# Performance work log

Hardware: AMD Instinct MI355X
Metric: run time of the kernel (lower is better)

## Reference

```python
import jax, jax.numpy as jnp
import numpy as np

R, N, F, H, C = 3, 100000, 256, 128, 2
N0, S1, D1, S2, D2 = 16384, 16384, 4096, 4096, 512


def setup_inputs() -> dict:
    key = jax.random.key(0)
    ks = jax.random.split(key, 13)
    return {
        "features": jax.random.normal(ks[0], (N, F), jnp.float32),
        "src_nodes": jax.random.randint(ks[1], (R, N0), 0, N),
        "dstsrc2src1": jax.random.randint(ks[2], (R, S1), 0, N0),
        "dstsrc2dst1": jax.random.randint(ks[3], (R, D1), 0, N0),
        "dif_mat1": jax.random.uniform(ks[4], (R, D1, S1), jnp.float32) / S1,
        "dstsrc2src2": jax.random.randint(ks[5], (R, S2), 0, D1),
        "dstsrc2dst2": jax.random.randint(ks[6], (R, D2), 0, D1),
        "dif_mat2": jax.random.uniform(ks[7], (R, D2, S2), jnp.float32) / S2,
        "w1": jax.random.normal(ks[8], (2 * F, H), jnp.float32) * 0.05,
        "w2": jax.random.normal(ks[9], (2 * H, H), jnp.float32) * 0.05,
        "relation_vectors": jax.random.uniform(ks[10], (R, H), jnp.float32),
        "attention_vec": jax.random.uniform(ks[11], (2 * H, 1), jnp.float32),
        "classifier_w": jax.random.normal(ks[12], (H, C), jnp.float32) * 0.05,
    }


def _agg(x, d2s, d2d, dif, w, rel_vec, att_vec):
    # x: [n, din]; dif: [d, s]; w: [2*din, H]
    agg = dif @ x[d2s]                                  # mean-diffused neighbor feats [d, din]
    h = jnp.concatenate([agg, x[d2d]], axis=1) @ w      # [d, H]
    rel = jnp.broadcast_to(rel_vec[None, :], (h.shape[0], rel_vec.shape[0]))
    score = (jnp.concatenate([h, rel], axis=1) @ att_vec)[:, 0]  # [d]
    att = jax.nn.softmax(score)                         # softmax over batch nodes
    return h * att[:, None]


def reference(features, src_nodes, dstsrc2src1, dstsrc2dst1, dif_mat1,
              dstsrc2src2, dstsrc2dst2, dif_mat2, w1, w2,
              relation_vectors, attention_vec, classifier_w):
    def per_relation(src, s1, d1, m1, s2, d2, m2, rel_vec):
        x = features[src]                               # gather node feats [N0, F]
        x = _agg(x, s1, d1, m1, w1, rel_vec, attention_vec)   # [D1, H]
        x = _agg(x, s2, d2, m2, w2, rel_vec, attention_vec)   # [D2, H]
        return x

    xs = jax.vmap(per_relation)(src_nodes, dstsrc2src1, dstsrc2dst1, dif_mat1,
                                dstsrc2src2, dstsrc2dst2, dif_mat2, relation_vectors)
    summed = jnp.sum(xs, axis=0)                        # sum over relations [D2, H]
    inv_norm = jax.lax.rsqrt(jnp.maximum(jnp.sum(summed * summed, axis=1, keepdims=True), 1e-12))
    normed = summed * inv_norm                          # tf.nn.l2_normalize(axis=1)
    return jax.nn.softmax(normed @ classifier_w, axis=-1)
```

## Files before the change

### kernel.cpp

```cpp
#include <hip/hip_runtime.h>
#include <hip/hip_bf16.h>
#include <math.h>

constexpr int Rc  = 3;
constexpr int Fc  = 256;
constexpr int Hc  = 128;
constexpr int N0c = 16384;
constexpr int S1c = 16384;
constexpr int D1c = 4096;
constexpr int S2c = 4096;
constexpr int D2c = 512;
constexpr int KH1 = 4;
constexpr int KH2 = 16;

typedef __bf16 bf16x8 __attribute__((ext_vector_type(8)));
typedef __bf16 bf16x4 __attribute__((ext_vector_type(4)));
typedef float  f32x4  __attribute__((ext_vector_type(4)));

__device__ __forceinline__ void glds16(const void* g, void* l) {
  __builtin_amdgcn_global_load_lds(
      (const __attribute__((address_space(1))) void*)g,
      (__attribute__((address_space(3))) void*)l, 16, 0, 0);
}

__device__ __forceinline__ bf16x8 cvt2(const float4 a, const float4 b) {
  bf16x8 c;
  c[0] = (__bf16)a.x; c[1] = (__bf16)a.y; c[2] = (__bf16)a.z; c[3] = (__bf16)a.w;
  c[4] = (__bf16)b.x; c[5] = (__bf16)b.y; c[6] = (__bf16)b.z; c[7] = (__bf16)b.w;
  return c;
}

__device__ __forceinline__ unsigned short bfbits(float v) {
  __bf16 b = (__bf16)v; unsigned short u;
  __builtin_memcpy(&u, &b, 2); return u;
}

__global__ __launch_bounds__(256, 2)
void wpack(const float* __restrict__ w1, const float* __restrict__ w2,
           unsigned char* __restrict__ wp, float* __restrict__ esum) {
  const int tile = blockIdx.x, half = blockIdx.y, t = threadIdx.x;
  if (tile == 0 && half == 0 && t < 8) esum[t] = 0.f;
  const float* src; int row0;
  if (tile < 4)       { src = w1; row0 = tile * 64; }
  else if (tile < 8)  { src = w1; row0 = 256 + (tile - 4) * 64; }
  else if (tile < 10) { src = w2; row0 = (tile - 8) * 64; }
  else                { src = w2; row0 = 128 + (tile - 10) * 64; }
  unsigned char* dst = wp + ((size_t)half * 12 + tile) * 16384;
  __shared__ float sm[64][132];
  {
    const int r = t >> 2, c0 = (t & 3) * 32;
#pragma unroll
    for (int j = 0; j < 8; j++)
      *(float4*)&sm[r][c0 + 4 * j] = *(const float4*)(src + (size_t)(row0 + r) * 128 + c0 + 4 * j);
  }
  __syncthreads();
  if (t < 128) {
    const int n = t;
#pragma unroll
    for (int ch = 0; ch < 8; ch++) {
      bf16x8 o;
#pragma unroll
      for (int e = 0; e < 8; e++) {
        float v = sm[ch * 8 + e][n];
        __bf16 h = (__bf16)v;
        o[e] = half ? (__bf16)(v - (float)h) : h;
      }
      *(bf16x8*)(dst + n * 128 + ((ch ^ (n & 7)) * 16)) = o;
    }
  }
}

__global__ __launch_bounds__(256, 3)
void gg0(const float* __restrict__ feat, const int* __restrict__ srcn,
         const int* __restrict__ d2s1, const unsigned char* __restrict__ wp,
         unsigned char* __restrict__ xgwp) {
  const int rel = blockIdx.y, bx = blockIdx.x, s0 = bx * 64;
  const unsigned char* Bh = wp;
  const unsigned char* Bl = wp + (size_t)12 * 16384;

  const int t = threadIdx.x, lane = t & 63, w = t >> 6;
  const int mh = w >> 1, nh = w & 1;

  __shared__ __bf16 Asm[64 * 64];
  __shared__ __bf16 Bhs[128 * 64];
  __shared__ __bf16 Bls[128 * 64];

  const int arow = t >> 2, ak0 = (t & 3) * 16;
  const int row = s0 + arow;
  const size_t arowg = (size_t)srcn[rel * N0c + d2s1[(size_t)rel * S1c + row]];
  const float* aptr = feat + arowg * Fc + ak0;
  const int ac0 = ak0 >> 3;
  __bf16* asw0 = &Asm[arow * 64 + ((ac0    ) ^ (arow & 7)) * 8];
  __bf16* asw1 = &Asm[arow * 64 + ((ac0 + 1) ^ (arow & 7)) * 8];

  float4 a[16];
#pragma unroll
  for (int tl = 0; tl < 4; tl++)
#pragma unroll
    for (int j = 0; j < 4; j++) a[tl * 4 + j] = *(const float4*)(aptr + tl * 64 + 4 * j);

  f32x4 acc[2][4] = {};

  for (int tl = 0; tl < 4; ++tl) {
    asm volatile("s_waitcnt lgkmcnt(0)" ::: "memory");
    __builtin_amdgcn_s_barrier();
    __builtin_amdgcn_sched_barrier(0);
    {
      const unsigned char* bh = Bh + (size_t)tl * 16384 + w * 4096 + lane * 16;
      const unsigned char* bl = Bl + (size_t)tl * 16384 + w * 4096 + lane * 16;
      char* dh = (char*)Bhs + w * 4096;
      char* dl = (char*)Bls + w * 4096;
#pragma unroll
      for (int i = 0; i < 4; i++) glds16(bh + i * 1024, dh + i * 1024);
#pragma unroll
      for (int i = 0; i < 4; i++) glds16(bl + i * 1024, dl + i * 1024);
    }
    *(bf16x8*)asw0 = cvt2(a[tl * 4 + 0], a[tl * 4 + 1]);
    *(bf16x8*)asw1 = cvt2(a[tl * 4 + 2], a[tl * 4 + 3]);
    asm volatile("s_waitcnt vmcnt(0) lgkmcnt(0)" ::: "memory");
    __builtin_amdgcn_s_barrier();
    __builtin_amdgcn_sched_barrier(0);
#pragma unroll
    for (int ks = 0; ks < 2; ks++) {
      const int ch = ks * 4 + (lane >> 4);
      bf16x8 af[2], bh[4], bl[4];
#pragma unroll
      for (int mi = 0; mi < 2; mi++) {
        int r = mh * 32 + mi * 16 + (lane & 15);
        af[mi] = *(const bf16x8*)&Asm[r * 64 + ((ch ^ (r & 7)) * 8)];
      }
#pragma unroll
      for (int ni = 0; ni < 4; ni++) {
        int n = nh * 64 + ni * 16 + (lane & 15);
        bh[ni] = *(const bf16x8*)&Bhs[n * 64 + ((ch ^ (n & 7)) * 8)];
        bl[ni] = *(const bf16x8*)&Bls[n * 64 + ((ch ^ (n & 7)) * 8)];
      }
#pragma unroll
      for (int mi = 0; mi < 2; mi++)
#pragma unroll
        for (int ni = 0; ni < 4; ni++) {
          acc[mi][ni] = __builtin_amdgcn_mfma_f32_16x16x32_bf16(af[mi], bh[ni], acc[mi][ni], 0, 0, 0);
          acc[mi][ni] = __builtin_amdgcn_mfma_f32_16x16x32_bf16(af[mi], bl[ni], acc[mi][ni], 0, 0, 0);
        }
    }
  }
  unsigned char* tile = xgwp + ((size_t)(rel * (S1c >> 6) + bx)) * 16384;
#pragma unroll
  for (int mi = 0; mi < 2; mi++)
#pragma unroll
    for (int ni = 0; ni < 4; ni++) {
      const int sl0 = mh * 32 + mi * 16 + (lane >> 4) * 4;
      const int n = nh * 64 + ni * 16 + (lane & 15);
      const int ch = sl0 >> 3, e0 = sl0 & 7, cs = ch ^ (n & 7);
      ushort4 u;
      u.x = bfbits(acc[mi][ni][0]); u.y = bfbits(acc[mi][ni][1]);
      u.z = bfbits(acc[mi][ni][2]); u.w = bfbits(acc[mi][ni][3]);
      *(ushort4*)(tile + n * 128 + cs * 16 + e0 * 2) = u;
    }
}

__global__ __launch_bounds__(256, 3)
void big1p(const float* __restrict__ dif1, const unsigned char* __restrict__ xgwp,
           float* __restrict__ aggP, const float* __restrict__ feat,
           const int* __restrict__ srcn, const int* __restrict__ d2d1,
           const unsigned char* __restrict__ wp, float* __restrict__ xdw) {
  __shared__ char lds[49152];
  const int t = threadIdx.x, lane = t & 63, w = t >> 6;
  const int mh = w >> 1, nh = w & 1;

  if (blockIdx.x < 768) {
    __bf16* Abuf = (__bf16*)lds;
    __bf16* Bbuf = (__bf16*)(lds + 16384);
    const int F = blockIdx.x;
    const int xcd = F & 7, r = F >> 3;
    const int sub = r >> 5, m = r & 31;
    const int h = xcd + 8 * sub;
    const int g2 = h >> 1;
    const int rel = g2 >> 2, kh = g2 & 3;
    const int m0 = ((h & 1) * 32 + m) * 64;
    constexpr int NP = 64;
    constexpr int NM = 32;

    const unsigned char* Bt = xgwp + ((size_t)rel * 256 + (size_t)kh * NP) * 16384;
    float* Cg = aggP + (((size_t)kh * Rc + rel) * D1c + m0) * 128;

    const int lst = (lane & 31) >> 4;
    const int lr2 = lane >> 5;
    const int fo  = (lane & 31) * 4;
    const int ch  = (fo & 63) >> 3;
    const int eo  = fo & 7;
    const float* aW = dif1 + ((size_t)(rel * D1c + m0 + w * 16 + lr2)) * S1c
                    + (size_t)kh * 4096 + fo;
    const unsigned char* bsrc = Bt + w * 4096 + lane * 16;

    f32x4 acc[2][4] = {};
    f32x4 a0[8], a1[8];

#define LOAD_A(ARR, M_) do { _Pragma("unroll") \
    for (int ri = 0; ri < 8; ri++) \
      ARR[ri] = __builtin_nontemporal_load( \
          (const f32x4*)(aW + (size_t)ri * 2 * S1c + (size_t)(M_) * 128)); \
  } while (0)

#define WRITE_A(ARR, NBUF) do { if (lst == (NBUF)) { _Pragma("unroll") \
    for (int ri = 0; ri < 8; ri++) { \
      const int row_ = w * 16 + ri * 2 + lr2; \
      bf16x4 cv_; \
      cv_[0] = (__bf16)ARR[ri].x; cv_[1] = (__bf16)ARR[ri].y; \
      cv_[2] = (__bf16)ARR[ri].z; cv_[3] = (__bf16)ARR[ri].w; \
      *(bf16x4*)&Abuf[(NBUF) * 4096 + row_ * 64 + ((ch ^ (row_ & 7)) * 8) + eo] = cv_; \
    } } } while (0)

    LOAD_A(a0, 0);
    {
      char* bd = (char*)Bbuf + w * 4096;
#pragma unroll
      for (int i = 0; i < 4; i++) glds16(bsrc + i * 1024, bd + i * 1024);
    }
    WRITE_A(a0, 0);
    LOAD_A(a1, 1);

#pragma unroll 1
    for (int g = 0; g < NP; ++g) {
      const int buf = g & 1, nbuf = buf ^ 1;
      asm volatile("s_waitcnt lgkmcnt(0)" ::: "memory");
      __builtin_amdgcn_s_barrier();
      __builtin_amdgcn_sched_barrier(0);
      if (g + 1 < NP) {
        const unsigned char* bs = bsrc + (size_t)(g + 1) * 16384;
        char* bd = (char*)Bbuf + nbuf * 16384 + w * 4096;
#pragma unroll
        for (int i = 0; i < 4; i++) glds16(bs + i * 1024, bd + i * 1024);
      }
      if (g + 1 < NP) {
        const int mw = (g + 1) >> 1;
        if ((mw & 1) == 0) { WRITE_A(a0, nbuf); }
        else               { WRITE_A(a1, nbuf); }
      }
      if (g & 1) {
        const int mn = (g + 3) >> 1;
        if (mn < NM) {
          if ((mn & 1) == 0) { LOAD_A(a0, mn); }
          else               { LOAD_A(a1, mn); }
        }
      }
      if (g < NP - 2)
        asm volatile("s_waitcnt vmcnt(12) lgkmcnt(0)" ::: "memory");
      else if (g == NP - 2)
        asm volatile("s_waitcnt vmcnt(4) lgkmcnt(0)" ::: "memory");
      else
        asm volatile("s_waitcnt vmcnt(0) lgkmcnt(0)" ::: "memory");
      __builtin_amdgcn_s_barrier();
      __builtin_amdgcn_sched_barrier(0);
      const __bf16* Ac = Abuf + buf * 4096;
      const __bf16* Bc = Bbuf + buf * 8192;
#pragma unroll
      for (int ks = 0; ks < 2; ks++) {
        const int cch = ks * 4 + (lane >> 4);
        bf16x8 af[2], bfr[4];
#pragma unroll
        for (int mi = 0; mi < 2; mi++) {
          int rr = mh * 32 + mi * 16 + (lane & 15);
          af[mi] = *(const bf16x8*)&Ac[rr * 64 + ((cch ^ (rr & 7)) * 8)];
        }
#pragma unroll
        for (int ni = 0; ni < 4; ni++) {
          int n = nh * 64 + ni * 16 + (lane & 15);
          bfr[ni] = *(const bf16x8*)&Bc[n * 64 + ((cch ^ (n & 7)) * 8)];
        }
#pragma unroll
        for (int mi = 0; mi < 2; mi++)
#pragma unroll
          for (int ni = 0; ni < 4; ni++)
            acc[mi][ni] = __builtin_amdgcn_mfma_f32_16x16x32_bf16(af[mi], bfr[ni], acc[mi][ni], 0, 0, 0);
      }
    }
#undef LOAD_A
#undef WRITE_A
#pragma unroll
    for (int mi = 0; mi < 2; mi++)
#pragma unroll
      for (int ni = 0; ni < 4; ni++) {
        const int col = nh * 64 + ni * 16 + (lane & 15);
#pragma unroll
        for (int j = 0; j < 4; j++) {
          const int rr = mh * 32 + mi * 16 + (lane >> 4) * 4 + j;
          Cg[(size_t)rr * 128 + col] = acc[mi][ni][j];
        }
      }
  } else {
    __bf16* Asm = (__bf16*)lds;
    __bf16* Bhs = (__bf16*)(lds + 8192);
    __bf16* Bls = (__bf16*)(lds + 24576);
    const int jb = blockIdx.x - 768;
    const int rel = jb >> 6, bx = jb & 63, s0 = bx * 64;
    const unsigned char* Bh = wp + (size_t)4 * 16384;
    const unsigned char* Bl = wp + (size_t)16 * 16384;

    const int arow = t >> 2, ak0 = (t & 3) * 16;
    const int row = s0 + arow;
    const size_t arowg = (size_t)srcn[rel * N0c + d2d1[(size_t)rel * D1c + row]];
    const float* aptr = feat + arowg * Fc + ak0;
    const int ac0 = ak0 >> 3;
    __bf16* asw0 = &Asm[arow * 64 + ((ac0    ) ^ (arow & 7)) * 8];
    __bf16* asw1 = &Asm[arow * 64 + ((ac0 + 1) ^ (arow & 7)) * 8];

    float4 a[16];
#pragma unroll
    for (int tl = 0; tl < 4; tl++)
#pragma unroll
      for (int j = 0; j < 4; j++) a[tl * 4 + j] = *(const float4*)(aptr + tl * 64 + 4 * j);

    f32x4 acc[2][4] = {};
    for (int tl = 0; tl < 4; ++tl) {
      asm volatile("s_waitcnt lgkmcnt(0)" ::: "memory");
      __builtin_amdgcn_s_barrier();
      __builtin_amdgcn_sched_barrier(0);
      {
        const unsigned char* bh = Bh + (size_t)tl * 16384 + w * 4096 + lane * 16;
        const unsigned char* bl = Bl + (size_t)tl * 16384 + w * 4096 + lane * 16;
        char* dh = (char*)Bhs + w * 4096;
        char* dl = (char*)Bls + w * 4096;
#pragma unroll
        for (int i = 0; i < 4; i++) glds16(bh + i * 1024, dh + i * 1024);
#pragma unroll
        for (int i = 0; i < 4; i++) glds16(bl + i * 1024, dl + i * 1024);
      }
      *(bf16x8*)asw0 = cvt2(a[tl * 4 + 0], a[tl * 4 + 1]);
      *(bf16x8*)asw1 = cvt2(a[tl * 4 + 2], a[tl * 4 + 3]);
      asm volatile("s_waitcnt vmcnt(0) lgkmcnt(0)" ::: "memory");
      __builtin_amdgcn_s_barrier();
      __builtin_amdgcn_sched_barrier(0);
#pragma unroll
      for (int ks = 0; ks < 2; ks++) {
        const int ch = ks * 4 + (lane >> 4);
        bf16x8 af[2], bh[4], bl[4];
#pragma unroll
        for (int mi = 0; mi < 2; mi++) {
          int r = mh * 32 + mi * 16 + (lane & 15);
          af[mi] = *(const bf16x8*)&Asm[r * 64 + ((ch ^ (r & 7)) * 8)];
        }
#pragma unroll
        for (int ni = 0; ni < 4; ni++) {
          int n = nh * 64 + ni * 16 + (lane & 15);
          bh[ni] = *(const bf16x8*)&Bhs[n * 64 + ((ch ^ (n & 7)) * 8)];
          bl[ni] = *(const bf16x8*)&Bls[n * 64 + ((ch ^ (n & 7)) * 8)];
        }
#pragma unroll
        for (int mi = 0; mi < 2; mi++)
#pragma unroll
          for (int ni = 0; ni < 4; ni++) {
            acc[mi][ni] = __builtin_amdgcn_mfma_f32_16x16x32_bf16(af[mi], bh[ni], acc[mi][ni], 0, 0, 0);
            acc[mi][ni] = __builtin_amdgcn_mfma_f32_16x16x32_bf16(af[mi], bl[ni], acc[mi][ni], 0, 0, 0);
          }
      }
    }
#pragma unroll
    for (int mi = 0; mi < 2; mi++)
#pragma unroll
      for (int ni = 0; ni < 4; ni++) {
        const int col = nh * 64 + ni * 16 + (lane & 15);
#pragma unroll
        for (int j = 0; j < 4; j++) {
          const int rr = mh * 32 + mi * 16 + (lane >> 4) * 4 + j;
          xdw[((size_t)rel * D1c + s0 + rr) * 128 + col] = acc[mi][ni][j];
        }
      }
  }
}

__global__ __launch_bounds__(256, 3)
void gemm_big(const float* __restrict__ A, const unsigned char* __restrict__ Bp,
              float* __restrict__ C, int M, int KTOT, int KH) {
  const int rel = blockIdx.z, kh = blockIdx.y, m0 = blockIdx.x * 64;
  const int t = threadIdx.x, lane = t & 63, w = t >> 6;
  const int KB = KTOT / KH, NT = KB >> 6;
  const int mh = w >> 1, nh = w & 1;

  const float* Ag = A + ((size_t)rel * M + m0) * KTOT + (size_t)kh * KB;
  const unsigned char* Bt = Bp + ((size_t)rel * (KTOT >> 6) + (size_t)kh * NT) * 16384;
  float* Cg = C + (((size_t)kh * Rc + rel) * M + m0) * 128;

  __shared__ __bf16 Asm[64 * 64];
  __shared__ __bf16 Bsm[2][128 * 64];

  f32x4 acc[2][4] = {};
  const int arow = t >> 2, ak0 = (t & 3) * 16;
  const float* aptr = Ag + (size_t)arow * KTOT + ak0;
  const int ac0 = ak0 >> 3;
  __bf16* asw0 = &Asm[arow * 64 + ((ac0    ) ^ (arow & 7)) * 8];
  __bf16* asw1 = &Asm[arow * 64 + ((ac0 + 1) ^ (arow & 7)) * 8];
  const unsigned char* bsrc = Bt + w * 4096 + lane * 16;

  float4 a0[4], a1[4];
#pragma unroll
  for (int j = 0; j < 4; j++) a0[j] = *(const float4*)(aptr + 4 * j);
  {
    char* bd = (char*)Bsm[0] + w * 4096;
#pragma unroll
    for (int i = 0; i < 4; i++) glds16(bsrc + i * 1024, bd + i * 1024);
  }

  for (int tl = 0; tl < NT; ++tl) {
    const int cur = tl & 1;
    asm volatile("s_waitcnt lgkmcnt(0)" ::: "memory");
    __builtin_amdgcn_s_barrier();
    __builtin_amdgcn_sched_barrier(0);
    if (tl + 1 < NT) {
      const unsigned char* bs = bsrc + (size_t)(tl + 1) * 16384;
      char* bd = (char*)Bsm[cur ^ 1] + w * 4096;
#pragma unroll
      for (int i = 0; i < 4; i++) glds16(bs + i * 1024, bd + i * 1024);
      const float* ap = aptr + (size_t)(tl + 1) * 64;
#pragma unroll
      for (int j = 0; j < 4; j++) a1[j] = *(const float4*)(ap + 4 * j);
    }
    *(bf16x8*)asw0 = cvt2(a0[0], a0[1]);
    *(bf16x8*)asw1 = cvt2(a0[2], a0[3]);
    if (tl + 1 < NT)
      asm volatile("s_waitcnt vmcnt(8) lgkmcnt(0)" ::: "memory");
    else
      asm volatile("s_waitcnt vmcnt(0) lgkmcnt(0)" ::: "memory");
    __builtin_amdgcn_s_barrier();
    __builtin_amdgcn_sched_barrier(0);
    const __bf16* Bc = Bsm[cur];
#pragma unroll
    for (int ks = 0; ks < 2; ks++) {
      const int ch = ks * 4 + (lane >> 4);
      bf16x8 af[2], bfr[4];
#pragma unroll
      for (int mi = 0; mi < 2; mi++) {
        int r = mh * 32 + mi * 16 + (lane & 15);
        af[mi] = *(const bf16x8*)&Asm[r * 64 + ((ch ^ (r & 7)) * 8)];
      }
#pragma unroll
      for (int ni = 0; ni < 4; ni++) {
        int n = nh * 64 + ni * 16 + (lane & 15);
        bfr[ni] = *(const bf16x8*)&Bc[n * 64 + ((ch ^ (n & 7)) * 8)];
      }
#pragma unroll
      for (int mi = 0; mi < 2; mi++)
#pragma unroll
        for (int ni = 0; ni < 4; ni++)
          acc[mi][ni] = __builtin_amdgcn_mfma_f32_16x16x32_bf16(af[mi], bfr[ni], acc[mi][ni], 0, 0, 0);
    }
#pragma unroll
    for (int j = 0; j < 4; j++) a0[j] = a1[j];
  }
#pragma unroll
  for (int mi = 0; mi < 2; mi++)
#pragma unroll
    for (int ni = 0; ni < 4; ni++) {
      const int col = nh * 64 + ni * 16 + (lane & 15);
#pragma unroll
      for (int j = 0; j < 4; j++) {
        const int r = mh * 32 + mi * 16 + (lane >> 4) * 4 + j;
        Cg[(size_t)r * 128 + col] = acc[mi][ni][j];
      }
    }
}

__global__ __launch_bounds__(256, 3)
void c1_l2(const float* __restrict__ aggP, const float* __restrict__ xdw,
           const float* __restrict__ attv, const unsigned char* __restrict__ wp,
           float* __restrict__ escore1, float* __restrict__ esum,
           float* __restrict__ P, float* __restrict__ Q) {
  const int rel = blockIdx.y, d0 = blockIdx.x * 64;
  const int t = threadIdx.x, lane = t & 63, w = t >> 6;
  const int mh = w >> 1, nh = w & 1;

  __shared__ __bf16 Asm[64 * 128];
  __shared__ __bf16 Bhs[128 * 64];
  __shared__ __bf16 Bls[128 * 64];
  __shared__ float  sred[64];

  const int r = t >> 2, c0 = (t & 3) * 32;
  float4 x0[8];
  {
    const size_t base = ((size_t)rel * D1c + d0 + r) * 128 + c0;
#pragma unroll
    for (int j = 0; j < 8; j++) x0[j] = *(const float4*)(xdw + base + 4 * j);
#pragma unroll
    for (int p2 = 0; p2 < KH1; p2++) {
      const float* ap = aggP + (((size_t)p2 * Rc + rel) * D1c + d0 + r) * 128 + c0;
#pragma unroll
      for (int j = 0; j < 8; j++) {
        float4 u = *(const float4*)(ap + 4 * j);
        x0[j].x += u.x; x0[j].y += u.y; x0[j].z += u.z; x0[j].w += u.w;
      }
    }
  }
  float sp = 0.f;
#pragma unroll
  for (int j = 0; j < 8; j++) {
    sp += x0[j].x * attv[c0 + 4 * j]     + x0[j].y * attv[c0 + 4 * j + 1]
        + x0[j].z * attv[c0 + 4 * j + 2] + x0[j].w * attv[c0 + 4 * j + 3];
  }
  sp += __shfl_xor(sp, 1); sp += __shfl_xor(sp, 2);
  const float e = expf(sp);
  if ((t & 3) == 0) { escore1[(size_t)rel * D1c + d0 + r] = e; sred[r] = e; }
  const int ch0 = (t & 3) * 4;
#pragma unroll
  for (int q = 0; q < 4; q++) {
    *(bf16x8*)&Asm[r * 128 + (((ch0 + q) ^ (r & 7)) * 8)] = cvt2(x0[2 * q], x0[2 * q + 1]);
  }
  __syncthreads();
  if (t < 64) {
    float v = sred[t];
    v += __shfl_down(v, 32); v += __shfl_down(v, 16); v += __shfl_down(v, 8);
    v += __shfl_down(v, 4);  v += __shfl_down(v, 2);  v += __shfl_down(v, 1);
    if (t == 0) atomicAdd(esum + rel, v);
  }
  f32x4 accP[2][4] = {}, accQ[2][4] = {};
#pragma unroll
  for (int z = 0; z < 2; z++) {
#pragma unroll
    for (int tl = 0; tl < 2; tl++) {
      if (!(z == 0 && tl == 0)) {
        asm volatile("s_waitcnt lgkmcnt(0)" ::: "memory");
        __builtin_amdgcn_s_barrier();
        __builtin_amdgcn_sched_barrier(0);
      }
      {
        const unsigned char* bh = wp + (size_t)(8 + z * 2 + tl) * 16384 + w * 4096 + lane * 16;
        const unsigned char* bl = wp + (size_t)(20 + z * 2 + tl) * 16384 + w * 4096 + lane * 16;
        char* dh = (char*)Bhs + w * 4096;
        char* dl = (char*)Bls + w * 4096;
#pragma unroll
        for (int i = 0; i < 4; i++) glds16(bh + i * 1024, dh + i * 1024);
#pragma unroll
        for (int i = 0; i < 4; i++) glds16(bl + i * 1024, dl + i * 1024);
      }
      asm volatile("s_waitcnt vmcnt(0) lgkmcnt(0)" ::: "memory");
      __builtin_amdgcn_s_barrier();
      __builtin_amdgcn_sched_barrier(0);
      f32x4 (*acc)[4] = z ? accQ : accP;
#pragma unroll
      for (int ks = 0; ks < 2; ks++) {
        const int lch = ks * 4 + (lane >> 4);
        const int ch  = tl * 8 + lch;
        bf16x8 af[2], bh[4], bl[4];
#pragma unroll
        for (int mi = 0; mi < 2; mi++) {
          int rr = mh * 32 + mi * 16 + (lane & 15);
          af[mi] = *(const bf16x8*)&Asm[rr * 128 + ((ch ^ (rr & 7)) * 8)];
        }
#pragma unroll
        for (int ni = 0; ni < 4; ni++) {
          int n = nh * 64 + ni * 16 + (lane & 15);
          bh[ni] = *(const bf16x8*)&Bhs[n * 64 + ((lch ^ (n & 7)) * 8)];
          bl[ni] = *(const bf16x8*)&Bls[n * 64 + ((lch ^ (n & 7)) * 8)];
        }
#pragma unroll
        for (int mi = 0; mi < 2; mi++)
#pragma unroll
          for (int ni = 0; ni < 4; ni++) {
            acc[mi][ni] = __builtin_amdgcn_mfma_f32_16x16x32_bf16(af[mi], bh[ni], acc[mi][ni], 0, 0, 0);
            acc[mi][ni] = __builtin_amdgcn_mfma_f32_16x16x32_bf16(af[mi], bl[ni], acc[mi][ni], 0, 0, 0);
          }
      }
    }
  }
#pragma unroll
  for (int mi = 0; mi < 2; mi++)
#pragma unroll
    for (int ni = 0; ni < 4; ni++) {
      const int col = nh * 64 + ni * 16 + (lane & 15);
#pragma unroll
      for (int j = 0; j < 4; j++) {
        const int rr = mh * 32 + mi * 16 + (lane >> 4) * 4 + j;
        P[((size_t)rel * D1c + d0 + rr) * 128 + col] = accP[mi][ni][j];
        Q[((size_t)rel * D1c + d0 + rr) * 128 + col] = accQ[mi][ni][j];
      }
    }
}

__global__ __launch_bounds__(256, 2)
void pgpack(const float* __restrict__ P, const int* __restrict__ d2s2,
            const float* __restrict__ escore1, const float* __restrict__ esum,
            unsigned char* __restrict__ PGp) {
  const int rel = blockIdx.y, kb = blockIdx.x, t = threadIdx.x;
  const float inv1 = 1.0f / esum[rel];
  __shared__ __bf16 sm[64][136];
  {
    const int kl = t >> 2, c0 = (t & 3) * 32;
    const int sr = d2s2[rel * S2c + kb * 64 + kl];
    const float sc = escore1[(size_t)rel * D1c + sr] * inv1;
    const float4* p = (const float4*)(P + ((size_t)rel * D1c + sr) * 128 + c0);
#pragma unroll
    for (int j = 0; j < 4; j++) {
      float4 v0 = p[2 * j], v1 = p[2 * j + 1];
      v0.x *= sc; v0.y *= sc; v0.z *= sc; v0.w *= sc;
      v1.x *= sc; v1.y *= sc; v1.z *= sc; v1.w *= sc;
      *(bf16x8*)&sm[kl][c0 + 8 * j] = cvt2(v0, v1);
    }
  }
  __syncthreads();
  if (t < 128) {
    const int n = t;
    unsigned char* dst = PGp + ((size_t)(rel * (S2c >> 6) + kb)) * 16384;
#pragma unroll
    for (int ch = 0; ch < 8; ch++) {
      bf16x8 o;
#pragma unroll
      for (int e = 0; e < 8; e++) o[e] = sm[ch * 8 + e][n];
      *(bf16x8*)(dst + n * 128 + ((ch ^ (n & 7)) * 16)) = o;
    }
  }
}

__global__ __launch_bounds__(128, 4)
void combine2(const float* __restrict__ aggP2, const float* __restrict__ Q,
              const int* __restrict__ d2d2, const float* __restrict__ attv,
              const float* __restrict__ escore1, const float* __restrict__ esum,
              float* __restrict__ h2, float* __restrict__ escore2) {
  const int rel = blockIdx.y, d0 = blockIdx.x * 8, t = threadIdx.x;
  const float inv1 = 1.0f / esum[rel];
  float acc[8];
#pragma unroll
  for (int i = 0; i < 8; i++) {
    const int d = d0 + i;
    const int qr = d2d2[rel * D2c + d];
    const float qs = escore1[(size_t)rel * D1c + qr] * inv1;
    float v = Q[((size_t)rel * D1c + qr) * 128 + t] * qs;
#pragma unroll
    for (int p = 0; p < KH2; p++)
      v += aggP2[(((size_t)p * Rc + rel) * D2c + d) * 128 + t];
    acc[i] = v;
    h2[((size_t)rel * D2c + d) * 128 + t] = v;
  }
  const float avt = attv[t];
  __shared__ float sred[2][8];
#pragma unroll
  for (int i = 0; i < 8; i++) {
    float p = acc[i] * avt;
    p += __shfl_down(p, 32); p += __shfl_down(p, 16); p += __shfl_down(p, 8);
    p += __shfl_down(p, 4);  p += __shfl_down(p, 2);  p += __shfl_down(p, 1);
    if ((t & 63) == 0) sred[t >> 6][i] = p;
  }
  __syncthreads();
  if (t < 8) {
    const float e2 = expf(sred[0][t] + sred[1][t]);
    escore2[rel * D2c + d0 + t] = e2;
    float v = e2;
    v += __shfl_down(v, 4); v += __shfl_down(v, 2); v += __shfl_down(v, 1);
    if (t == 0) atomicAdd((float*)esum + 4 + rel, v);
  }
}

__global__ __launch_bounds__(128, 4)
void k9_final(const float* __restrict__ h2, const float* __restrict__ escore2,
              const float* __restrict__ esum, const float* __restrict__ cw,
              float* __restrict__ out) {
  const int d = blockIdx.x, t = threadIdx.x;
  float v = 0.f;
#pragma unroll
  for (int r = 0; r < Rc; r++) {
    const float att = escore2[r * D2c + d] / esum[4 + r];
    v += h2[((size_t)r * D2c + d) * Hc + t] * att;
  }
  float ss = v * v;
  ss += __shfl_down(ss, 32); ss += __shfl_down(ss, 16); ss += __shfl_down(ss, 8);
  ss += __shfl_down(ss, 4);  ss += __shfl_down(ss, 2);  ss += __shfl_down(ss, 1);
  __shared__ float sr[3][2];
  if ((t & 63) == 0) sr[0][t >> 6] = ss;
  __syncthreads();
  const float tot = sr[0][0] + sr[0][1];
  const float inv = rsqrtf(fmaxf(tot, 1e-12f));
  const float nv = v * inv;
  float p0 = nv * cw[t * 2], p1 = nv * cw[t * 2 + 1];
  p0 += __shfl_down(p0, 32); p0 += __shfl_down(p0, 16); p0 += __shfl_down(p0, 8);
  p0 += __shfl_down(p0, 4);  p0 += __shfl_down(p0, 2);  p0 += __shfl_down(p0, 1);
  p1 += __shfl_down(p1, 32); p1 += __shfl_down(p1, 16); p1 += __shfl_down(p1, 8);
  p1 += __shfl_down(p1, 4);  p1 += __shfl_down(p1, 2);  p1 += __shfl_down(p1, 1);
  if ((t & 63) == 0) { sr[1][t >> 6] = p0; sr[2][t >> 6] = p1; }
  __syncthreads();
  if (t == 0) {
    const float l0 = sr[1][0] + sr[1][1];
    const float l1 = sr[2][0] + sr[2][1];
    const float m = fmaxf(l0, l1);
    const float e0 = expf(l0 - m), e1 = expf(l1 - m);
    const float is = 1.0f / (e0 + e1);
    out[d * 2 + 0] = e0 * is;
    out[d * 2 + 1] = e1 * is;
  }
}

extern "C" void kernel_launch(void* const* d_in, const int* in_sizes, int n_in,
                              void* d_out, int out_size, void* d_ws, size_t ws_size,
                              hipStream_t stream) {
  (void)in_sizes; (void)n_in; (void)out_size; (void)ws_size;
  const float* feat = (const float*)d_in[0];
  const int*   srcn = (const int*)d_in[1];
  const int*   d2s1 = (const int*)d_in[2];
  const int*   d2d1 = (const int*)d_in[3];
  const float* dif1 = (const float*)d_in[4];
  const int*   d2s2 = (const int*)d_in[5];
  const int*   d2d2 = (const int*)d_in[6];
  const float* dif2 = (const float*)d_in[7];
  const float* w1   = (const float*)d_in[8];
  const float* w2   = (const float*)d_in[9];
  const float* attv = (const float*)d_in[11];
  const float* cw   = (const float*)d_in[12];
  float* out = (float*)d_out;

  char* p = (char*)d_ws;
  auto take = [&](size_t n) { char* r = p; p += (n + 255) & ~(size_t)255; return r; };
  unsigned char* wp   = (unsigned char*)take(24 * 16384);
  unsigned char* xgwp = (unsigned char*)take((size_t)Rc * 256 * 16384);
  float* xdw    = (float*)take((size_t)Rc * D1c * 128 * 4);
  float* aggP   = (float*)take((size_t)KH1 * Rc * D1c * 128 * 4);
  float* escore1= (float*)take((size_t)Rc * D1c * 4);
  float* esum   = (float*)take(256);
  unsigned char* PGp = (unsigned char*)take((size_t)Rc * 64 * 16384);
  float* h2     = (float*)take((size_t)Rc * D2c * 128 * 4);
  float* escore2= (float*)take((size_t)Rc * D2c * 4);
  float* P = (float*)xgwp;
  float* Q = P + (size_t)Rc * D1c * 128;
  float* aggP2 = aggP;

  wpack<<<dim3(12, 2), 256, 0, stream>>>(w1, w2, wp, esum);
  gg0<<<dim3(256, Rc), 256, 0, stream>>>(feat, srcn, d2s1, wp, xgwp);
  big1p<<<960, 256, 0, stream>>>(dif1, xgwp, aggP, feat, srcn, d2d1, wp, xdw);
  c1_l2<<<dim3(D1c / 64, Rc), 256, 0, stream>>>(aggP, xdw, attv, wp, escore1, esum, P, Q);
  pgpack<<<dim3(S2c / 64, Rc), 256, 0, stream>>>(P, d2s2, escore1, esum, PGp);
  gemm_big<<<dim3(D2c / 64, KH2, Rc), 256, 0, stream>>>(dif2, PGp, aggP2, D2c, S2c, KH2);
  combine2<<<dim3(D2c / 8, Rc), 128, 0, stream>>>(aggP2, Q, d2d2, attv, escore1, esum, h2, escore2);
  k9_final<<<D2c, 128, 0, stream>>>(h2, escore2, esum, cw, out);
}
```

Before: 263.1 us.

## Double-buffer c1_l2 weight tiles, add nontemporal loads, halve combine2 rows per block

c1_l2 now prefetches its weight tiles into double-buffered LDS, issuing the first tile before the activation loads so copies overlap the MFMA work. Its launch bound drops to one block per SM because of the larger shared memory. gemm_big, c1_l2 and combine2 stream their fp32 partial-sum inputs with nontemporal loads to avoid polluting cache. combine2 handles 4 destination rows per block instead of 8, doubling the grid for more parallelism. Lower occupancy in c1_l2 may offset the overlap gain.

```diff
diff --git a/kernel.cpp b/kernel.cpp
--- a/kernel.cpp
+++ b/kernel.cpp
@@ -24,6 +24,13 @@
 }
 
 __device__ __forceinline__ bf16x8 cvt2(const float4 a, const float4 b) {
+  bf16x8 c;
+  c[0] = (__bf16)a.x; c[1] = (__bf16)a.y; c[2] = (__bf16)a.z; c[3] = (__bf16)a.w;
+  c[4] = (__bf16)b.x; c[5] = (__bf16)b.y; c[6] = (__bf16)b.z; c[7] = (__bf16)b.w;
+  return c;
+}
+
+__device__ __forceinline__ bf16x8 cvt2v(const f32x4 a, const f32x4 b) {
   bf16x8 c;
   c[0] = (__bf16)a.x; c[1] = (__bf16)a.y; c[2] = (__bf16)a.z; c[3] = (__bf16)a.w;
   c[4] = (__bf16)b.x; c[5] = (__bf16)b.y; c[6] = (__bf16)b.z; c[7] = (__bf16)b.w;
@@ -392,9 +399,9 @@
   __bf16* asw1 = &Asm[arow * 64 + ((ac0 + 1) ^ (arow & 7)) * 8];
   const unsigned char* bsrc = Bt + w * 4096 + lane * 16;
 
-  float4 a0[4], a1[4];
-#pragma unroll
-  for (int j = 0; j < 4; j++) a0[j] = *(const float4*)(aptr + 4 * j);
+  f32x4 a0[4], a1[4];
+#pragma unroll
+  for (int j = 0; j < 4; j++) a0[j] = __builtin_nontemporal_load((const f32x4*)(aptr + 4 * j));
   {
     char* bd = (char*)Bsm[0] + w * 4096;
 #pragma unroll
@@ -413,10 +420,10 @@
       for (int i = 0; i < 4; i++) glds16(bs + i * 1024, bd + i * 1024);
       const float* ap = aptr + (size_t)(tl + 1) * 64;
 #pragma unroll
-      for (int j = 0; j < 4; j++) a1[j] = *(const float4*)(ap + 4 * j);
-    }
-    *(bf16x8*)asw0 = cvt2(a0[0], a0[1]);
-    *(bf16x8*)asw1 = cvt2(a0[2], a0[3]);
+      for (int j = 0; j < 4; j++) a1[j] = __builtin_nontemporal_load((const f32x4*)(ap + 4 * j));
+    }
+    *(bf16x8*)asw0 = cvt2v(a0[0], a0[1]);
+    *(bf16x8*)asw1 = cvt2v(a0[2], a0[3]);
     if (tl + 1 < NT)
       asm volatile("s_waitcnt vmcnt(8) lgkmcnt(0)" ::: "memory");
     else
@@ -460,7 +467,7 @@
     }
 }
 
-__global__ __launch_bounds__(256, 3)
+__global__ __launch_bounds__(256, 1)
 void c1_l2(const float* __restrict__ aggP, const float* __restrict__ xdw,
            const float* __restrict__ attv, const unsigned char* __restrict__ wp,
            float* __restrict__ escore1, float* __restrict__ esum,
@@ -470,23 +477,35 @@
   const int mh = w >> 1, nh = w & 1;
 
   __shared__ __bf16 Asm[64 * 128];
-  __shared__ __bf16 Bhs[128 * 64];
-  __shared__ __bf16 Bls[128 * 64];
+  __shared__ __bf16 Bhs[2][128 * 64];
+  __shared__ __bf16 Bls[2][128 * 64];
   __shared__ float  sred[64];
 
+  {
+    const unsigned char* bh = wp + (size_t)8 * 16384 + w * 4096 + lane * 16;
+    const unsigned char* bl = wp + (size_t)20 * 16384 + w * 4096 + lane * 16;
+    char* dh = (char*)Bhs[0] + w * 4096;
+    char* dl = (char*)Bls[0] + w * 4096;
+#pragma unroll
+    for (int i = 0; i < 4; i++) glds16(bh + i * 1024, dh + i * 1024);
+#pragma unroll
+    for (int i = 0; i < 4; i++) glds16(bl + i * 1024, dl + i * 1024);
+  }
+
   const int r = t >> 2, c0 = (t & 3) * 32;
-  float4 x0[8];
+  f32x4 x0[8];
   {
     const size_t base = ((size_t)rel * D1c + d0 + r) * 128 + c0;
 #pragma unroll
-    for (int j = 0; j < 8; j++) x0[j] = *(const float4*)(xdw + base + 4 * j);
+    for (int j = 0; j < 8; j++)
+      x0[j] = __builtin_nontemporal_load((const f32x4*)(xdw + base + 4 * j));
 #pragma unroll
     for (int p2 = 0; p2 < KH1; p2++) {
       const float* ap = aggP + (((size_t)p2 * Rc + rel) * D1c + d0 + r) * 128 + c0;
 #pragma unroll
       for (int j = 0; j < 8; j++) {
-        float4 u = *(const float4*)(ap + 4 * j);
-        x0[j].x += u.x; x0[j].y += u.y; x0[j].z += u.z; x0[j].w += u.w;
+        f32x4 u = __builtin_nontemporal_load((const f32x4*)(ap + 4 * j));
+        x0[j] += u;
       }
     }
   }
@@ -502,7 +521,7 @@
   const int ch0 = (t & 3) * 4;
 #pragma unroll
   for (int q = 0; q < 4; q++) {
-    *(bf16x8*)&Asm[r * 128 + (((ch0 + q) ^ (r & 7)) * 8)] = cvt2(x0[2 * q], x0[2 * q + 1]);
+    *(bf16x8*)&Asm[r * 128 + (((ch0 + q) ^ (r & 7)) * 8)] = cvt2v(x0[2 * q], x0[2 * q + 1]);
   }
   __syncthreads();
   if (t < 64) {
@@ -511,54 +530,57 @@
     v += __shfl_down(v, 4);  v += __shfl_down(v, 2);  v += __shfl_down(v, 1);
     if (t == 0) atomicAdd(esum + rel, v);
   }
+
   f32x4 accP[2][4] = {}, accQ[2][4] = {};
 #pragma unroll
-  for (int z = 0; z < 2; z++) {
-#pragma unroll
-    for (int tl = 0; tl < 2; tl++) {
-      if (!(z == 0 && tl == 0)) {
-        asm volatile("s_waitcnt lgkmcnt(0)" ::: "memory");
-        __builtin_amdgcn_s_barrier();
-        __builtin_amdgcn_sched_barrier(0);
-      }
-      {
-        const unsigned char* bh = wp + (size_t)(8 + z * 2 + tl) * 16384 + w * 4096 + lane * 16;
-        const unsigned char* bl = wp + (size_t)(20 + z * 2 + tl) * 16384 + w * 4096 + lane * 16;
-        char* dh = (char*)Bhs + w * 4096;
-        char* dl = (char*)Bls + w * 4096;
-#pragma unroll
-        for (int i = 0; i < 4; i++) glds16(bh + i * 1024, dh + i * 1024);
-#pragma unroll
-        for (int i = 0; i < 4; i++) glds16(bl + i * 1024, dl + i * 1024);
-      }
-      asm volatile("s_waitcnt vmcnt(0) lgkmcnt(0)" ::: "memory");
+  for (int p = 0; p < 4; ++p) {
+    const int buf = p & 1;
+    if (p) {
+      asm volatile("s_waitcnt lgkmcnt(0)" ::: "memory");
       __builtin_amdgcn_s_barrier();
       __builtin_amdgcn_sched_barrier(0);
-      f32x4 (*acc)[4] = z ? accQ : accP;
-#pragma unroll
-      for (int ks = 0; ks < 2; ks++) {
-        const int lch = ks * 4 + (lane >> 4);
-        const int ch  = tl * 8 + lch;
-        bf16x8 af[2], bh[4], bl[4];
-#pragma unroll
-        for (int mi = 0; mi < 2; mi++) {
-          int rr = mh * 32 + mi * 16 + (lane & 15);
-          af[mi] = *(const bf16x8*)&Asm[rr * 128 + ((ch ^ (rr & 7)) * 8)];
-        }
+    }
+    if (p < 3) {
+      const unsigned char* bh = wp + (size_t)(8 + p + 1) * 16384 + w * 4096 + lane * 16;
+      const unsigned char* bl = wp + (size_t)(20 + p + 1) * 16384 + w * 4096 + lane * 16;
+      char* dh = (char*)Bhs[buf ^ 1] + w * 4096;
+      char* dl = (char*)Bls[buf ^ 1] + w * 4096;
+#pragma unroll
+      for (int i = 0; i < 4; i++) glds16(bh + i * 1024, dh + i * 1024);
+#pragma unroll
+      for (int i = 0; i < 4; i++) glds16(bl + i * 1024, dl + i * 1024);
+    }
+    if (p < 3)
+      asm volatile("s_waitcnt vmcnt(8) lgkmcnt(0)" ::: "memory");
+    else
+      asm volatile("s_waitcnt vmcnt(0) lgkmcnt(0)" ::: "memory");
+    __builtin_amdgcn_s_barrier();
+    __builtin_amdgcn_sched_barrier(0);
+    const int z = p >> 1, tl = p & 1;
+    f32x4 (*acc)[4] = z ? accQ : accP;
+#pragma unroll
+    for (int ks = 0; ks < 2; ks++) {
+      const int lch = ks * 4 + (lane >> 4);
+      const int ch  = tl * 8 + lch;
+      bf16x8 af[2], bh[4], bl[4];
+#pragma unroll
+      for (int mi = 0; mi < 2; mi++) {
+        int rr = mh * 32 + mi * 16 + (lane & 15);
+        af[mi] = *(const bf16x8*)&Asm[rr * 128 + ((ch ^ (rr & 7)) * 8)];
+      }
+#pragma unroll
+      for (int ni = 0; ni < 4; ni++) {
+        int n = nh * 64 + ni * 16 + (lane & 15);
+        bh[ni] = *(const bf16x8*)&Bhs[buf][n * 64 + ((lch ^ (n & 7)) * 8)];
+        bl[ni] = *(const bf16x8*)&Bls[buf][n * 64 + ((lch ^ (n & 7)) * 8)];
+      }
+#pragma unroll
+      for (int mi = 0; mi < 2; mi++)
 #pragma unroll
         for (int ni = 0; ni < 4; ni++) {
-          int n = nh * 64 + ni * 16 + (lane & 15);
-          bh[ni] = *(const bf16x8*)&Bhs[n * 64 + ((lch ^ (n & 7)) * 8)];
-          bl[ni] = *(const bf16x8*)&Bls[n * 64 + ((lch ^ (n & 7)) * 8)];
-        }
-#pragma unroll
-        for (int mi = 0; mi < 2; mi++)
-#pragma unroll
-          for (int ni = 0; ni < 4; ni++) {
-            acc[mi][ni] = __builtin_amdgcn_mfma_f32_16x16x32_bf16(af[mi], bh[ni], acc[mi][ni], 0, 0, 0);
-            acc[mi][ni] = __builtin_amdgcn_mfma_f32_16x16x32_bf16(af[mi], bl[ni], acc[mi][ni], 0, 0, 0);
-          }
-      }
+          acc[mi][ni] = __builtin_amdgcn_mfma_f32_16x16x32_bf16(af[mi], bh[ni], acc[mi][ni], 0, 0, 0);
+          acc[mi][ni] = __builtin_amdgcn_mfma_f32_16x16x32_bf16(af[mi], bl[ni], acc[mi][ni], 0, 0, 0);
+        }
     }
   }
 #pragma unroll
@@ -614,36 +636,37 @@
               const int* __restrict__ d2d2, const float* __restrict__ attv,
               const float* __restrict__ escore1, const float* __restrict__ esum,
               float* __restrict__ h2, float* __restrict__ escore2) {
-  const int rel = blockIdx.y, d0 = blockIdx.x * 8, t = threadIdx.x;
+  const int rel = blockIdx.y, d0 = blockIdx.x * 4, t = threadIdx.x;
   const float inv1 = 1.0f / esum[rel];
-  float acc[8];
-#pragma unroll
-  for (int i = 0; i < 8; i++) {
+  float acc[4];
+#pragma unroll
+  for (int i = 0; i < 4; i++) {
     const int d = d0 + i;
     const int qr = d2d2[rel * D2c + d];
     const float qs = escore1[(size_t)rel * D1c + qr] * inv1;
     float v = Q[((size_t)rel * D1c + qr) * 128 + t] * qs;
 #pragma unroll
     for (int p = 0; p < KH2; p++)
-      v += aggP2[(((size_t)p * Rc + rel) * D2c + d) * 128 + t];
+      v += __builtin_nontemporal_load(
+          &aggP2[(((size_t)p * Rc + rel) * D2c + d) * 128 + t]);
     acc[i] = v;
     h2[((size_t)rel * D2c + d) * 128 + t] = v;
   }
   const float avt = attv[t];
-  __shared__ float sred[2][8];
-#pragma unroll
-  for (int i = 0; i < 8; i++) {
+  __shared__ float sred[2][4];
+#pragma unroll
+  for (int i = 0; i < 4; i++) {
     float p = acc[i] * avt;
     p += __shfl_down(p, 32); p += __shfl_down(p, 16); p += __shfl_down(p, 8);
     p += __shfl_down(p, 4);  p += __shfl_down(p, 2);  p += __shfl_down(p, 1);
     if ((t & 63) == 0) sred[t >> 6][i] = p;
   }
   __syncthreads();
-  if (t < 8) {
+  if (t < 4) {
     const float e2 = expf(sred[0][t] + sred[1][t]);
     escore2[rel * D2c + d0 + t] = e2;
     float v = e2;
-    v += __shfl_down(v, 4); v += __shfl_down(v, 2); v += __shfl_down(v, 1);
+    v += __shfl_down(v, 2); v += __shfl_down(v, 1);
     if (t == 0) atomicAdd((float*)esum + 4 + rel, v);
   }
 }
@@ -725,6 +748,6 @@
   c1_l2<<<dim3(D1c / 64, Rc), 256, 0, stream>>>(aggP, xdw, attv, wp, escore1, esum, P, Q);
   pgpack<<<dim3(S2c / 64, Rc), 256, 0, stream>>>(P, d2s2, escore1, esum, PGp);
   gemm_big<<<dim3(D2c / 64, KH2, Rc), 256, 0, stream>>>(dif2, PGp, aggP2, D2c, S2c, KH2);
-  combine2<<<dim3(D2c / 8, Rc), 128, 0, stream>>>(aggP2, Q, d2d2, attv, escore1, esum, h2, escore2);
+  combine2<<<dim3(D2c / 4, Rc), 128, 0, stream>>>(aggP2, Q, d2d2, attv, escore1, esum, h2, escore2);
   k9_final<<<D2c, 128, 0, stream>>>(h2, escore2, esum, cw, out);
 }
```

Result: no change. 268.3 us (+2.0%).
